# Kernel tuning notes

Hardware: AMD Instinct MI355X
Metric: run time of the kernel (lower is better)

Reference implementation:

```python
import jax, jax.numpy as jnp
import numpy as np
from jax import lax

# LNS semantics: values are held as (sign, log_base|x|); exact conversion round-trips
# make log-domain mul/add mathematically identical to float conv/linear/relu, so the
# faithful reference is the equivalent float pipeline.

def _conv(x, w, b):
    # x: [B,C,H,W], w: [O,C,kh,kw] (torch layout), stride 1, no padding
    y = lax.conv_general_dilated(x, w, window_strides=(1, 1), padding='VALID',
                                 dimension_numbers=('NCHW', 'OIHW', 'NCHW'))
    return y + b[None, :, None, None]

def _maxpool2(x):
    return lax.reduce_window(x, -jnp.inf, lax.max,
                             window_dimensions=(1, 1, 2, 2),
                             window_strides=(1, 1, 2, 2), padding='VALID')

def setup_inputs() -> dict:
    key = jax.random.key(0)
    ks = jax.random.split(key, 9)
    s = lambda k, shape, fan: jax.random.normal(k, shape, jnp.float32) * (1.0 / np.sqrt(fan))
    return {
        'x': jax.random.normal(ks[0], (512, 1, 54, 54), jnp.float32),
        'conv1_w': s(ks[1], (32, 1, 3, 3), 9),
        'conv1_b': s(ks[2], (32,), 9),
        'conv2_w': s(ks[3], (64, 32, 3, 3), 32 * 9),
        'conv2_b': s(ks[4], (64,), 32 * 9),
        'fc1_w': s(ks[5], (128, 9216), 9216),
        'fc1_b': s(ks[6], (128,), 9216),
        'fc2_w': s(ks[7], (10, 128), 128),
        'fc2_b': s(ks[8], (10,), 128),
    }

def reference(x, conv1_w, conv1_b, conv2_w, conv2_b, fc1_w, fc1_b, fc2_w, fc2_b):
    h = jnp.maximum(_conv(x, conv1_w, conv1_b), 0.0)          # [B,32,52,52]
    h = _maxpool2(h)                                          # [B,32,26,26]
    h = jnp.maximum(_conv(h, conv2_w, conv2_b), 0.0)          # [B,64,24,24]
    h = _maxpool2(h)                                          # [B,64,12,12]
    h = h.reshape(h.shape[0], -1)                             # [B,9216]
    h = jnp.maximum(h @ fc1_w.T + fc1_b, 0.0)                 # [B,128]
    return h @ fc2_w.T + fc2_b                                # [B,10]
```

## Files before the change

### kernel.cpp

```cpp
#include <hip/hip_runtime.h>


#define B 512
#define POS 676
#define ICP 36
#define P2SZ (64*12*12)
#define SCR 26

typedef unsigned short ushort_t;
typedef ushort_t ushort4v __attribute__((ext_vector_type(4)));
typedef short s16x8 __attribute__((ext_vector_type(8)));
typedef float f32x4 __attribute__((ext_vector_type(4)));
typedef float f32x2 __attribute__((ext_vector_type(2)));

__device__ __forceinline__ ushort_t f2bf(float f) {
    union { float f; unsigned u; } a; a.f = f;
    unsigned r = a.u + 0x7FFFu + ((a.u >> 16) & 1u);
    return (ushort_t)(r >> 16);
}
__device__ __forceinline__ float bf2f(ushort_t u) {
    union { unsigned u; float f; } a; a.u = ((unsigned)u) << 16;
    return a.f;
}

#define N_WR (64 * 9 * 32)
#define N_WF (128 * 9216)
#define CONV1_BLOCKS 3328
#define PREP_BLOCKS  4680

__global__ __launch_bounds__(256) void conv1_prep(const float* __restrict__ x,
                                                  const float* __restrict__ w,
                                                  const float* __restrict__ bias,
                                                  const float* __restrict__ c2w,
                                                  const float* __restrict__ f1w,
                                                  ushort_t* __restrict__ out,
                                                  ushort_t* __restrict__ wr,
                                                  ushort_t* __restrict__ wfb) {
    int blk = blockIdx.x;
    if (blk >= CONV1_BLOCKS) {
        int t = (blk - CONV1_BLOCKS) * 256 + threadIdx.x;
        if (t < N_WR) {
            int ic  = t & 31;
            int tap = (t >> 5) % 9;
            int oc  = t / 288;
            wr[t] = f2bf(c2w[oc * 288 + ic * 9 + tap]);
        } else if (t < N_WR + N_WF) {
            int i  = t - N_WR;
            int oc  = i & 63;
            int pos = (i >> 6) % 144;
            int n   = i / 9216;
            wfb[i] = f2bf(f1w[(size_t)n * 9216 + oc * 144 + pos]);
        }
        return;
    }
    int t = blk * 256 + threadIdx.x;
    int ic = t & 31;
    int r  = t >> 5;
    int h  = r & 1;
    int r2 = r >> 1;
    int py = r2 % 26;
    int b  = r2 / 26;
    int px0 = h * 13;

    const float* wp = w + ic * 9;
    float w00 = wp[0], w01 = wp[1], w02 = wp[2];
    float w10 = wp[3], w11 = wp[4], w12 = wp[5];
    float w20 = wp[6], w21 = wp[7], w22 = wp[8];
    float bv = bias[ic];

    const float* xr = x + b * (54 * 54) + (2 * py) * 54 + 2 * px0;
    ushort_t* po = out + ((size_t)b * POS + py * 26 + px0) * 32 + ic;

    f32x2 p[4], q[4];
#pragma unroll
    for (int rr = 0; rr < 4; ++rr) p[rr] = *reinterpret_cast<const f32x2*>(xr + rr * 54);
#pragma unroll
    for (int rr = 0; rr < 4; ++rr) q[rr] = *reinterpret_cast<const f32x2*>(xr + rr * 54 + 2);

#pragma unroll
    for (int j = 0; j < 13; ++j) {
        f32x2 mid[4];
#pragma unroll
        for (int rr = 0; rr < 4; ++rr) mid[rr] = (f32x2){p[rr].y, q[rr].x};

        f32x2 s0 = p[0] * (f32x2)w00 + mid[0] * (f32x2)w01 + q[0] * (f32x2)w02
                 + p[1] * (f32x2)w10 + mid[1] * (f32x2)w11 + q[1] * (f32x2)w12
                 + p[2] * (f32x2)w20 + mid[2] * (f32x2)w21 + q[2] * (f32x2)w22;
        f32x2 s1 = p[1] * (f32x2)w00 + mid[1] * (f32x2)w01 + q[1] * (f32x2)w02
                 + p[2] * (f32x2)w10 + mid[2] * (f32x2)w11 + q[2] * (f32x2)w12
                 + p[3] * (f32x2)w20 + mid[3] * (f32x2)w21 + q[3] * (f32x2)w22;

        float m = fmaxf(fmaxf(s0.x, s0.y), fmaxf(s1.x, s1.y));
        po[j * 32] = f2bf(fmaxf(m + bv, 0.0f));
        if (j < 12) {
#pragma unroll
            for (int rr = 0; rr < 4; ++rr) {
                p[rr] = q[rr];
                q[rr] = *reinterpret_cast<const f32x2*>(xr + rr * 54 + 2 * j + 4);
            }
        }
    }
}

__global__ __launch_bounds__(512) void conv2_mfma(const ushort_t* __restrict__ p1,
                                                  const ushort_t* __restrict__ wr,
                                                  const float* __restrict__ bias,
                                                  ushort_t* __restrict__ pool2cl) {
    __shared__ ushort_t lds[260 * ICP];
    int blk = blockIdx.x;
    int b = blk / 3, c = blk % 3;
    int tid = threadIdx.x;

    const ushort_t* src = p1 + ((size_t)b * POS + 8 * c * 26) * 32;
    for (int t = tid; t < 260 * 8; t += 512) {
        int pos = t >> 3, off = (t & 7) * 4;
        ushort4v v = *reinterpret_cast<const ushort4v*>(src + pos * 32 + off);
        *reinterpret_cast<ushort4v*>(&lds[pos * ICP + off]) = v;
    }
    __syncthreads();

    int lane = tid & 63, wid = tid >> 6;
    int quad = lane >> 4, lr = lane & 15;
    int prow = wid >> 1;
    int nhalf = wid & 1;

    int ebase[3];
#pragma unroll
    for (int t = 0; t < 3; ++t) {
        int m  = t * 16 + lr;
        int yl = m / 24;
        int xx = m - yl * 24;
        ebase[t] = ((2 * prow + yl) * 26 + xx) * ICP + quad * 8;
    }

    f32x4 acc[3][2];
#pragma unroll
    for (int t = 0; t < 3; ++t)
#pragma unroll
        for (int n = 0; n < 2; ++n) acc[t][n] = (f32x4){0.f, 0.f, 0.f, 0.f};

    const ushort_t* wb = wr + (size_t)(nhalf * 32 + lr) * 288 + quad * 8;

#pragma unroll
    for (int tap = 0; tap < 9; ++tap) {
        int ky = tap / 3, kx = tap % 3;
        int koff = (ky * 26 + kx) * ICP;
        s16x8 a[3];
#pragma unroll
        for (int t = 0; t < 3; ++t) {
            union { ushort4v s[2]; s16x8 v; } u;
            u.s[0] = *reinterpret_cast<const ushort4v*>(&lds[ebase[t] + koff]);
            u.s[1] = *reinterpret_cast<const ushort4v*>(&lds[ebase[t] + koff + 4]);
            a[t] = u.v;
        }
        s16x8 bf[2];
#pragma unroll
        for (int n = 0; n < 2; ++n)
            bf[n] = *reinterpret_cast<const s16x8*>(wb + (size_t)n * 16 * 288 + tap * 32);
#pragma unroll
        for (int t = 0; t < 3; ++t)
#pragma unroll
            for (int n = 0; n < 2; ++n)
                acc[t][n] = __builtin_amdgcn_mfma_f32_16x16x32_bf16(a[t], bf[n], acc[t][n], 0, 0, 0);
    }
    __syncthreads();

    ushort_t* scr = lds + wid * (32 * SCR);
#pragma unroll
    for (int t = 0; t < 3; ++t)
#pragma unroll
        for (int n = 0; n < 2; ++n) {
            int ocl = n * 16 + lr;
            int i0 = t * 8 + quad * 2;
            float v0 = fmaxf(acc[t][n][0], acc[t][n][1]);
            float v1 = fmaxf(acc[t][n][2], acc[t][n][3]);
            union { ushort_t u2[2]; unsigned w; } pk;
            pk.u2[0] = f2bf(v0); pk.u2[1] = f2bf(v1);
            *reinterpret_cast<unsigned*>(&scr[ocl * SCR + i0]) = pk.w;
        }
    int ocl = lane & 31;
    int pxh = lane >> 5;
    int oc  = nhalf * 32 + ocl;
    const ushort_t* row = scr + ocl * SCR;
    float bv = bias[oc];
    int py = c * 4 + prow;
    ushort_t* po = pool2cl + ((size_t)b * 144 + py * 12) * 64 + oc;
#pragma unroll
    for (int j = 0; j < 6; ++j) {
        int px = pxh * 6 + j;
        float r0 = bf2f(row[px]);
        float r1 = bf2f(row[px + 12]);
        po[px * 64] = f2bf(fmaxf(fmaxf(r0, r1) + bv, 0.0f));
    }
}

__global__ __launch_bounds__(256) void fc1_mfma(const ushort_t* __restrict__ A,
                                                 const ushort_t* __restrict__ W,
                                                 float* __restrict__ Cpart) {
    int tid = threadIdx.x;
    int lane = tid & 63, wid = tid >> 6;
    int lr = lane & 15, quad = lane >> 4;
    int w  = blockIdx.x * 4 + wid;
    int nt = w & 3;
    int ks = (w >> 2) & 31;
    int mt = w >> 7;

    int m0 = mt * 32;
    int n0 = nt * 32;
    int k0 = ks * 288 + quad * 8;
    const ushort_t* a0 = A + (size_t)(m0 + lr) * 9216 + k0;
    const ushort_t* a1 = a0 + (size_t)16 * 9216;
    const ushort_t* b0 = W + (size_t)(n0 + lr) * 9216 + k0;
    const ushort_t* b1 = b0 + (size_t)16 * 9216;

    f32x4 acc[2][2];
#pragma unroll
    for (int i = 0; i < 2; ++i)
#pragma unroll
        for (int j = 0; j < 2; ++j) acc[i][j] = (f32x4){0.f, 0.f, 0.f, 0.f};

#pragma unroll
    for (int kk = 0; kk < 9; ++kk) {
        s16x8 av0 = *reinterpret_cast<const s16x8*>(a0 + kk * 32);
        s16x8 av1 = *reinterpret_cast<const s16x8*>(a1 + kk * 32);
        s16x8 bv0 = *reinterpret_cast<const s16x8*>(b0 + kk * 32);
        s16x8 bv1 = *reinterpret_cast<const s16x8*>(b1 + kk * 32);
        acc[0][0] = __builtin_amdgcn_mfma_f32_16x16x32_bf16(av0, bv0, acc[0][0], 0, 0, 0);
        acc[0][1] = __builtin_amdgcn_mfma_f32_16x16x32_bf16(av0, bv1, acc[0][1], 0, 0, 0);
        acc[1][0] = __builtin_amdgcn_mfma_f32_16x16x32_bf16(av1, bv0, acc[1][0], 0, 0, 0);
        acc[1][1] = __builtin_amdgcn_mfma_f32_16x16x32_bf16(av1, bv1, acc[1][1], 0, 0, 0);
    }

    float* cp = Cpart + (size_t)ks * (512 * 128);
#pragma unroll
    for (int i = 0; i < 2; ++i) {
        int crow = m0 + i * 16 + quad * 4;
#pragma unroll
        for (int j = 0; j < 2; ++j) {
            int col = n0 + j * 16 + lr;
#pragma unroll
            for (int r = 0; r < 4; ++r)
                cp[(size_t)(crow + r) * 128 + col] = acc[i][j][r];
        }
    }
}

__global__ __launch_bounds__(128) void fc1fc2(const float* __restrict__ Cpart,
                                              const float* __restrict__ b1,
                                              const float* __restrict__ w2,
                                              const float* __restrict__ b2,
                                              float* __restrict__ out) {
    __shared__ float h[128];
    int b = blockIdx.x, k = threadIdx.x;
    float s = 0.f;
#pragma unroll
    for (int ks = 0; ks < 32; ++ks) s += Cpart[(size_t)ks * (512 * 128) + b * 128 + k];
    h[k] = fmaxf(s + b1[k], 0.0f);
    __syncthreads();
    if (k < 10) {
        const float* wp = w2 + k * 128;
        float acc = 0.f;
#pragma unroll 8
        for (int j = 0; j < 128; ++j) acc += h[j] * wp[j];
        out[b * 10 + k] = acc + b2[k];
    }
}

extern "C" void kernel_launch(void* const* d_in, const int* in_sizes, int n_in,
                              void* d_out, int out_size, void* d_ws, size_t ws_size,
                              hipStream_t stream) {
    const float* x       = (const float*)d_in[0];
    const float* conv1_w = (const float*)d_in[1];
    const float* conv1_b = (const float*)d_in[2];
    const float* conv2_w = (const float*)d_in[3];
    const float* conv2_b = (const float*)d_in[4];
    const float* fc1_w   = (const float*)d_in[5];
    const float* fc1_b   = (const float*)d_in[6];
    const float* fc2_w   = (const float*)d_in[7];
    const float* fc2_b   = (const float*)d_in[8];
    float* out = (float*)d_out;

    char* ws = (char*)d_ws;
    ushort_t* pool1 = (ushort_t*)ws;
    ws += (size_t)B * POS * 32 * sizeof(ushort_t);
    ushort_t* wr = (ushort_t*)ws;
    ws += N_WR * sizeof(ushort_t) + 128;
    ushort_t* wfb = (ushort_t*)ws;
    ws += N_WF * sizeof(ushort_t) + 128;
    ushort_t* pool2cl = (ushort_t*)ws;
    ws += (size_t)B * P2SZ * sizeof(ushort_t) + 128;
    float* Cpart = (float*)ws;
    ws += (size_t)32 * 512 * 128 * sizeof(float) + 128;

    conv1_prep<<<CONV1_BLOCKS + PREP_BLOCKS, 256, 0, stream>>>(
        x, conv1_w, conv1_b, conv2_w, fc1_w, pool1, wr, wfb);
    conv2_mfma<<<B * 3, 512, 0, stream>>>(pool1, wr, conv2_b, pool2cl);
    fc1_mfma<<<512, 256, 0, stream>>>(pool2cl, wfb, Cpart);
    fc1fc2<<<B, 128, 0, stream>>>(Cpart, fc1_b, fc2_w, fc2_b, out);
}
```

Before: 130.5 us.

## Coalesce fc1 weight transpose via LDS and halve fc1 split-K partials

The fc1 weight repack now uses a shared-memory tile per output row, so global reads and writes are coalesced instead of strided. The fc1 GEMM moves from 32 to 16 K splits with a 16-row M tile, which halves the partial-sum buffer written and then reduced. The reduction kernel handles two batch rows per block. The static LDS array is declared in the combined conv1 kernel, which may reduce occupancy for the conv1 blocks.

```diff
diff --git a/kernel.cpp b/kernel.cpp
--- a/kernel.cpp
+++ b/kernel.cpp
@@ -24,9 +24,9 @@
 }
 
 #define N_WR (64 * 9 * 32)
-#define N_WF (128 * 9216)
 #define CONV1_BLOCKS 3328
-#define PREP_BLOCKS  4680
+#define WR_BLOCKS 72
+#define TR_BLOCKS 128
 
 __global__ __launch_bounds__(256) void conv1_prep(const float* __restrict__ x,
                                                   const float* __restrict__ w,
@@ -36,24 +36,38 @@
                                                   ushort_t* __restrict__ out,
                                                   ushort_t* __restrict__ wr,
                                                   ushort_t* __restrict__ wfb) {
+    __shared__ float tr[64 * 145];
     int blk = blockIdx.x;
+    int tid = threadIdx.x;
+
+    if (blk >= CONV1_BLOCKS + WR_BLOCKS) {
+        int n = blk - CONV1_BLOCKS - WR_BLOCKS;
+        const float* src = f1w + (size_t)n * 9216;
+#pragma unroll
+        for (int i = 0; i < 36; ++i) {
+            int idx = i * 256 + tid;
+            int oc = idx / 144, pos = idx - oc * 144;
+            tr[oc * 145 + pos] = src[idx];
+        }
+        __syncthreads();
+        ushort_t* dst = wfb + (size_t)n * 9216;
+#pragma unroll
+        for (int i = 0; i < 36; ++i) {
+            int idx = i * 256 + tid;
+            int pos = idx >> 6, oc = idx & 63;
+            dst[idx] = f2bf(tr[oc * 145 + pos]);
+        }
+        return;
+    }
     if (blk >= CONV1_BLOCKS) {
-        int t = (blk - CONV1_BLOCKS) * 256 + threadIdx.x;
-        if (t < N_WR) {
-            int ic  = t & 31;
-            int tap = (t >> 5) % 9;
-            int oc  = t / 288;
-            wr[t] = f2bf(c2w[oc * 288 + ic * 9 + tap]);
-        } else if (t < N_WR + N_WF) {
-            int i  = t - N_WR;
-            int oc  = i & 63;
-            int pos = (i >> 6) % 144;
-            int n   = i / 9216;
-            wfb[i] = f2bf(f1w[(size_t)n * 9216 + oc * 144 + pos]);
-        }
+        int t = (blk - CONV1_BLOCKS) * 256 + tid;
+        int ic  = t & 31;
+        int tap = (t >> 5) % 9;
+        int oc  = t / 288;
+        wr[t] = f2bf(c2w[oc * 288 + ic * 9 + tap]);
         return;
     }
-    int t = blk * 256 + threadIdx.x;
+    int t = blk * 256 + tid;
     int ic = t & 31;
     int r  = t >> 5;
     int h  = r & 1;
@@ -202,66 +216,56 @@
     int lr = lane & 15, quad = lane >> 4;
     int w  = blockIdx.x * 4 + wid;
     int nt = w & 3;
-    int ks = (w >> 2) & 31;
-    int mt = w >> 7;
-
-    int m0 = mt * 32;
+    int ks = (w >> 2) & 15;
+    int mt = w >> 6;
+
+    int m0 = mt * 16;
     int n0 = nt * 32;
-    int k0 = ks * 288 + quad * 8;
+    int k0 = ks * 576 + quad * 8;
     const ushort_t* a0 = A + (size_t)(m0 + lr) * 9216 + k0;
-    const ushort_t* a1 = a0 + (size_t)16 * 9216;
     const ushort_t* b0 = W + (size_t)(n0 + lr) * 9216 + k0;
     const ushort_t* b1 = b0 + (size_t)16 * 9216;
 
-    f32x4 acc[2][2];
-#pragma unroll
-    for (int i = 0; i < 2; ++i)
-#pragma unroll
-        for (int j = 0; j < 2; ++j) acc[i][j] = (f32x4){0.f, 0.f, 0.f, 0.f};
-
-#pragma unroll
-    for (int kk = 0; kk < 9; ++kk) {
-        s16x8 av0 = *reinterpret_cast<const s16x8*>(a0 + kk * 32);
-        s16x8 av1 = *reinterpret_cast<const s16x8*>(a1 + kk * 32);
+    f32x4 acc0 = (f32x4){0.f, 0.f, 0.f, 0.f};
+    f32x4 acc1 = (f32x4){0.f, 0.f, 0.f, 0.f};
+
+#pragma unroll
+    for (int kk = 0; kk < 18; ++kk) {
+        s16x8 av  = *reinterpret_cast<const s16x8*>(a0 + kk * 32);
         s16x8 bv0 = *reinterpret_cast<const s16x8*>(b0 + kk * 32);
         s16x8 bv1 = *reinterpret_cast<const s16x8*>(b1 + kk * 32);
-        acc[0][0] = __builtin_amdgcn_mfma_f32_16x16x32_bf16(av0, bv0, acc[0][0], 0, 0, 0);
-        acc[0][1] = __builtin_amdgcn_mfma_f32_16x16x32_bf16(av0, bv1, acc[0][1], 0, 0, 0);
-        acc[1][0] = __builtin_amdgcn_mfma_f32_16x16x32_bf16(av1, bv0, acc[1][0], 0, 0, 0);
-        acc[1][1] = __builtin_amdgcn_mfma_f32_16x16x32_bf16(av1, bv1, acc[1][1], 0, 0, 0);
+        acc0 = __builtin_amdgcn_mfma_f32_16x16x32_bf16(av, bv0, acc0, 0, 0, 0);
+        acc1 = __builtin_amdgcn_mfma_f32_16x16x32_bf16(av, bv1, acc1, 0, 0, 0);
     }
 
     float* cp = Cpart + (size_t)ks * (512 * 128);
-#pragma unroll
-    for (int i = 0; i < 2; ++i) {
-        int crow = m0 + i * 16 + quad * 4;
-#pragma unroll
-        for (int j = 0; j < 2; ++j) {
-            int col = n0 + j * 16 + lr;
-#pragma unroll
-            for (int r = 0; r < 4; ++r)
-                cp[(size_t)(crow + r) * 128 + col] = acc[i][j][r];
-        }
-    }
-}
-
-__global__ __launch_bounds__(128) void fc1fc2(const float* __restrict__ Cpart,
+    int crow = m0 + quad * 4;
+#pragma unroll
+    for (int r = 0; r < 4; ++r) {
+        cp[(size_t)(crow + r) * 128 + n0 + lr]      = acc0[r];
+        cp[(size_t)(crow + r) * 128 + n0 + 16 + lr] = acc1[r];
+    }
+}
+
+__global__ __launch_bounds__(256) void fc1fc2(const float* __restrict__ Cpart,
                                               const float* __restrict__ b1,
                                               const float* __restrict__ w2,
                                               const float* __restrict__ b2,
                                               float* __restrict__ out) {
-    __shared__ float h[128];
-    int b = blockIdx.x, k = threadIdx.x;
+    __shared__ float h[2][128];
+    int half = threadIdx.x >> 7;
+    int k = threadIdx.x & 127;
+    int b = blockIdx.x * 2 + half;
     float s = 0.f;
 #pragma unroll
-    for (int ks = 0; ks < 32; ++ks) s += Cpart[(size_t)ks * (512 * 128) + b * 128 + k];
-    h[k] = fmaxf(s + b1[k], 0.0f);
+    for (int ks = 0; ks < 16; ++ks) s += Cpart[(size_t)ks * (512 * 128) + b * 128 + k];
+    h[half][k] = fmaxf(s + b1[k], 0.0f);
     __syncthreads();
     if (k < 10) {
         const float* wp = w2 + k * 128;
         float acc = 0.f;
 #pragma unroll 8
-        for (int j = 0; j < 128; ++j) acc += h[j] * wp[j];
+        for (int j = 0; j < 128; ++j) acc += h[half][j] * wp[j];
         out[b * 10 + k] = acc + b2[k];
     }
 }
@@ -286,15 +290,15 @@
     ushort_t* wr = (ushort_t*)ws;
     ws += N_WR * sizeof(ushort_t) + 128;
     ushort_t* wfb = (ushort_t*)ws;
-    ws += N_WF * sizeof(ushort_t) + 128;
+    ws += (size_t)128 * 9216 * sizeof(ushort_t) + 128;
     ushort_t* pool2cl = (ushort_t*)ws;
     ws += (size_t)B * P2SZ * sizeof(ushort_t) + 128;
     float* Cpart = (float*)ws;
-    ws += (size_t)32 * 512 * 128 * sizeof(float) + 128;
-
-    conv1_prep<<<CONV1_BLOCKS + PREP_BLOCKS, 256, 0, stream>>>(
+    ws += (size_t)16 * 512 * 128 * sizeof(float) + 128;
+
+    conv1_prep<<<CONV1_BLOCKS + WR_BLOCKS + TR_BLOCKS, 256, 0, stream>>>(
         x, conv1_w, conv1_b, conv2_w, fc1_w, pool1, wr, wfb);
     conv2_mfma<<<B * 3, 512, 0, stream>>>(pool1, wr, conv2_b, pool2cl);
     fc1_mfma<<<512, 256, 0, stream>>>(pool2cl, wfb, Cpart);
-    fc1fc2<<<B, 128, 0, stream>>>(Cpart, fc1_b, fc2_w, fc2_b, out);
-}
+    fc1fc2<<<256, 256, 0, stream>>>(Cpart, fc1_b, fc2_w, fc2_b, out);
+}
```

Result: no change. 131.8 us (+1.0%).
